# Kernel optimization log

Measured on AMD Instinct MI355X. Metric: run time of the kernel, lower is better.

## Reference

```python
import jax, jax.numpy as jnp
import numpy as np

BATCH, FIELD, EMB = 2048, 32, 64
LAYER_SIZES = [64, 64, 64]
OUT_DIM = 1
FINAL_DIM = sum(LAYER_SIZES)  # 192 (direct_connect=True, no splits)


def setup_inputs() -> dict:
    key = jax.random.key(0)
    ks = jax.random.split(key, 10)
    inp = {
        "x0": jax.random.normal(ks[0], (BATCH, FIELD, EMB), dtype=jnp.float32),
        # Conv1d(kernel_size=1) weights reshaped to (out, prev_field, field):
        "W1": jax.random.normal(ks[1], (LAYER_SIZES[0], FIELD, FIELD), dtype=jnp.float32) * 0.05,
        "b1": jax.random.normal(ks[2], (LAYER_SIZES[0],), dtype=jnp.float32) * 0.05,
        "W2": jax.random.normal(ks[3], (LAYER_SIZES[1], LAYER_SIZES[0], FIELD), dtype=jnp.float32) * 0.05,
        "b2": jax.random.normal(ks[4], (LAYER_SIZES[1],), dtype=jnp.float32) * 0.05,
        "W3": jax.random.normal(ks[5], (LAYER_SIZES[2], LAYER_SIZES[1], FIELD), dtype=jnp.float32) * 0.05,
        "b3": jax.random.normal(ks[6], (LAYER_SIZES[2],), dtype=jnp.float32) * 0.05,
        "W_out": jax.random.normal(ks[7], (FINAL_DIM, OUT_DIM), dtype=jnp.float32) * 0.05,
        "b_out": jax.random.normal(ks[8], (OUT_DIM,), dtype=jnp.float32) * 0.05,
    }
    return inp


def _cin_layer(W, b, xk, x0):
    # Fused: outer product einsum('bhd,bmd->bhmd') + reshape + 1x1 conv
    # == einsum over (prev_field h, field m) channel pair, per emb dim d.
    return jnp.einsum("ohm,bhd,bmd->bod", W, xk, x0) + b[None, :, None]


def reference(x0, W1, b1, W2, b2, W3, b3, W_out, b_out):
    # activation = identity; direct_connect = True (no splits, full carry)
    h1 = _cin_layer(W1, b1, x0, x0)   # (B, 64, D)
    h2 = _cin_layer(W2, b2, h1, x0)   # (B, 64, D)
    h3 = _cin_layer(W3, b3, h2, x0)   # (B, 64, D)
    stacked = jnp.concatenate([h1, h2, h3], axis=1)  # (B, 192, D)
    pooled = stacked.sum(axis=2)                     # (B, 192)
    return pooled @ W_out + b_out                    # (B, 1)
```

## Files before the change

kernel.cpp:

```cpp
#include <hip/hip_runtime.h>

typedef _Float16 f16;
typedef _Float16 f16x2 __attribute__((ext_vector_type(2)));
typedef __fp16 fp16x2 __attribute__((ext_vector_type(2)));
typedef _Float16 f16x8 __attribute__((ext_vector_type(8)));
typedef float f32x4 __attribute__((ext_vector_type(4)));
typedef unsigned int u32;

union U2 { u32 u; f16x2 h; fp16x2 h2; };
union AF { f16x8 v; u32 u[4]; };

__global__ __launch_bounds__(256) void pre_w3eff(
    const float* __restrict__ W3, const float* __restrict__ W_out,
    float* __restrict__ W3eff) {
    const int idx = blockIdx.x * 256 + threadIdx.x;
    float acc[8] = {0.f, 0.f, 0.f, 0.f, 0.f, 0.f, 0.f, 0.f};
#pragma unroll
    for (int ob = 0; ob < 8; ++ob)
#pragma unroll
        for (int oi = 0; oi < 8; ++oi) {
            int o = ob * 8 + oi;
            acc[oi] += W_out[128 + o] * W3[o * 2048 + idx];
        }
    float s = 0.f;
#pragma unroll
    for (int oi = 0; oi < 8; ++oi) s += acc[oi];
    W3eff[idx] = s;
}

__global__ __launch_bounds__(256) void pre_rest(
    const float* __restrict__ W1, const float* __restrict__ b1,
    const float* __restrict__ W2, const float* __restrict__ b2,
    const float* __restrict__ b3, const float* __restrict__ W_out,
    const float* __restrict__ b_out, const float* __restrict__ W3eff_g,
    f16* __restrict__ Wfrag, float* __restrict__ rvec, float* __restrict__ cnst) {
    const int blk = blockIdx.x, t = threadIdx.x;
    if (blk < 64) {
        const int h = blk;
        __shared__ float w3e[2048];
        __shared__ float w2s[2048];
        __shared__ float wo2[64];
#pragma unroll
        for (int i = 0; i < 8; ++i) {
            int idx = t + 256 * i;
            w3e[idx] = W3eff_g[idx];
            w2s[idx] = W2[((idx >> 5) * 64 + h) * 32 + (idx & 31)];
        }
        if (t < 64) wo2[t] = W_out[64 + t];
        __syncthreads();
        for (int idx = t; idx < 576; idx += 256) {
            int c = idx >> 5, kk = idx & 31;
            int sg = c >> 1, par = c & 1, A = kk >> 1, z = kk & 1;
            int B = (A + sg) & 15;
            float val = 0.f;
            if (sg == 0 && par == 1 && z == 1) {
                val = 0.f;
            } else if (sg == 8 && A >= 8) {
                int m = par ? (kk - 16) : kk;
                float s = 0.f;
#pragma unroll 8
                for (int o = 0; o < 64; ++o) s += wo2[o] * w2s[o * 32 + m];
                val = s;
            } else {
                int a = 2 * A + (par ? (1 - z) : z);
                int bq = 2 * B + z;
                float s = 0.f;
                if (a == bq) {
#pragma unroll 8
                    for (int o = 0; o < 64; ++o)
                        s += w3e[o * 32 + a] * w2s[o * 32 + a];
                } else {
#pragma unroll 8
                    for (int o = 0; o < 64; ++o)
                        s += w3e[o * 32 + bq] * w2s[o * 32 + a] +
                             w3e[o * 32 + a] * w2s[o * 32 + bq];
                }
                val = s;
            }
            int g = (kk >> 2) & 3, bb = (kk & 3) + 4 * (kk >> 4);
            int t4 = 4 + (h >> 4), l = 16 * g + (h & 15);
            Wfrag[((c * 8 + t4) * 64 + l) * 8 + bb] = (f16)val;
        }
    } else if (blk < 128) {
        const int h = blk - 64;
        __shared__ float w1r[1024];
        for (int i = t; i < 1024; i += 256) w1r[i] = W1[h * 1024 + i];
        __syncthreads();
        for (int idx = t; idx < 576; idx += 256) {
            int c = idx >> 5, kk = idx & 31;
            int sg = c >> 1, par = c & 1, A = kk >> 1, z = kk & 1;
            int B = (A + sg) & 15;
            float val = 0.f;
            if ((sg == 0 && par == 1 && z == 1) || (sg == 8 && A >= 8)) {
                val = 0.f;
            } else {
                int a = 2 * A + (par ? (1 - z) : z);
                int bq = 2 * B + z;
                val = (a == bq) ? w1r[33 * a] : (w1r[32 * a + bq] + w1r[32 * bq + a]);
            }
            int g = (kk >> 2) & 3, bb = (kk & 3) + 4 * (kk >> 4);
            int t4 = h >> 4, l = 16 * g + (h & 15);
            Wfrag[((c * 8 + t4) * 64 + l) * 8 + bb] = (f16)val;
        }
    } else {
        if (t < 32) {
            float acc[8] = {0.f, 0.f, 0.f, 0.f, 0.f, 0.f, 0.f, 0.f};
#pragma unroll
            for (int hb = 0; hb < 8; ++hb)
#pragma unroll
                for (int hi = 0; hi < 8; ++hi) {
                    int h = hb * 8 + hi;
                    acc[hi] += b2[h] * W3eff_g[h * 32 + t];
                }
            float r = 0.f;
#pragma unroll
            for (int hi = 0; hi < 8; ++hi) r += acc[hi];
            rvec[t] = r;
        }
        if (t >= 64 && t < 128) {
            int o = t - 64;
            float v = b1[o] * W_out[o] + b2[o] * W_out[64 + o] +
                      b3[o] * W_out[128 + o];
#pragma unroll
            for (int off = 32; off; off >>= 1) v += __shfl_xor(v, off);
            if (o == 0) cnst[0] = b_out[0] + 64.f * v;
        }
    }
}


#define EPOS(row, col) ((row) * 64 + (((col) + 4 * (row)) & 63))

__global__ __launch_bounds__(256, 3) void cin_main(
    const float* __restrict__ x0, const f16* __restrict__ Wfrag,
    const float* __restrict__ b1, const float* __restrict__ W_out,
    const float* __restrict__ rvec, const float* __restrict__ cnst,
    float* __restrict__ out) {
    __shared__ __align__(16) u32 FQ[2 * 32 * 130];
    __shared__ float eps[2][16 * 64];
    __shared__ float b1s[64], w1s[64], rs[32], rvb[2], obuf[2][2];

    const int t = threadIdx.x;
    const int w = t >> 6, lane = t & 63;
    const int wr = w >> 1, wc = w & 1;
    const int g = (lane >> 4) & 3, l15 = lane & 15;
    const int blk = blockIdx.x;

    {
        const float* src = x0 + (size_t)blk * 4096;
        const int J = t >> 4, l = t & 15;
        int r0 = 2 * J, r1 = 2 * J + 1, r2 = (2 * J + 2) & 31, r3 = (2 * J + 3) & 31;
#pragma unroll
        for (int bl = 0; bl < 2; ++bl) {
            const float* sb = src + bl * 2048;
#pragma unroll
            for (int k2 = 0; k2 < 4; ++k2) {
                int d = 16 * k2 + l;
                U2 u0, u1;
                u0.h2 = __builtin_amdgcn_cvt_pkrtz(sb[r0 * 64 + d], sb[r1 * 64 + d]);
                u1.h2 = __builtin_amdgcn_cvt_pkrtz(sb[r2 * 64 + d], sb[r3 * 64 + d]);
                uint2 ent; ent.x = u0.u; ent.y = u1.u;
                int base = bl * 4160 + J * 130 + 2 * d;
                *reinterpret_cast<uint2*>(&FQ[base]) = ent;
                *reinterpret_cast<uint2*>(&FQ[base + 2080]) = ent;
            }
        }
    }
    if (t < 64) { b1s[t] = b1[t]; w1s[t] = W_out[t]; }
    if (t >= 64 && t < 96) rs[t - 64] = rvec[t - 64];
    __syncthreads();

    const int v1base = wr * 4160 + 260 * g + 2 * l15;

    U2 xp[4][4], xpsw[4][4];
#pragma unroll
    for (int s = 0; s < 4; ++s) {
        uint2 qa = *reinterpret_cast<const uint2*>(&FQ[v1base + 32 * s]);
        uint2 qb = *reinterpret_cast<const uint2*>(&FQ[v1base + 32 * s + 1040]);
        xp[s][0].u = qa.x; xp[s][1].u = qa.y; xp[s][2].u = qb.x; xp[s][3].u = qb.y;
#pragma unroll
        for (int i = 0; i < 4; ++i)
            xpsw[s][i].u = (xp[s][i].u >> 16) | (xp[s][i].u << 16);
    }

    f32x4 acc[4][4];
#pragma unroll
    for (int s = 0; s < 4; ++s)
#pragma unroll
        for (int tt = 0; tt < 4; ++tt) acc[s][tt] = f32x4{0.f, 0.f, 0.f, 0.f};

    const f16x8* Wg = reinterpret_cast<const f16x8*>(Wfrag);
    f16x8 bfA[4], bfB[4];
#pragma unroll
    for (int tt = 0; tt < 4; ++tt) bfA[tt] = Wg[(wc * 4 + tt) * 64 + lane];

#define PKU(xa, ub) ({ U2 b_; b_.u = (ub); U2 r_; r_.h = (xa).h * b_.h; r_.u; })

#define PREF(dst, cc) { _Pragma("unroll") for (int tt = 0; tt < 4; ++tt) \
    dst[tt] = Wg[((cc) * 8 + wc * 4 + tt) * 64 + lane]; }

#define BODY(cc, bfr) { \
    _Pragma("unroll") \
    for (int s = 0; s < 4; ++s) { \
        AF af; \
        if ((cc) == 0) { \
            _Pragma("unroll") \
            for (int i = 0; i < 4; ++i) af.u[i] = PKU(xp[s][i], xp[s][i].u); \
        } else if ((cc) == 1) { \
            _Pragma("unroll") \
            for (int i = 0; i < 4; ++i) af.u[i] = PKU(xpsw[s][i], xp[s][i].u); \
        } else if ((cc) < 16) { \
            uint2 qa = *reinterpret_cast<const uint2*>(&FQ[v1base + 32 * s + ((cc) >> 1) * 130]); \
            uint2 qb = *reinterpret_cast<const uint2*>(&FQ[v1base + 32 * s + 1040 + ((cc) >> 1) * 130]); \
            if ((cc) & 1) { \
                af.u[0] = PKU(xpsw[s][0], qa.x); af.u[1] = PKU(xpsw[s][1], qa.y); \
                af.u[2] = PKU(xpsw[s][2], qb.x); af.u[3] = PKU(xpsw[s][3], qb.y); \
            } else { \
                af.u[0] = PKU(xp[s][0], qa.x); af.u[1] = PKU(xp[s][1], qa.y); \
                af.u[2] = PKU(xp[s][2], qb.x); af.u[3] = PKU(xp[s][3], qb.y); \
            } \
        } else if ((cc) == 16) { \
            uint2 qa = *reinterpret_cast<const uint2*>(&FQ[v1base + 32 * s + 1040]); \
            af.u[0] = PKU(xp[s][0], qa.x); af.u[1] = PKU(xp[s][1], qa.y); \
            af.u[2] = xp[s][2].u; af.u[3] = xp[s][3].u; \
        } else { \
            uint2 qa = *reinterpret_cast<const uint2*>(&FQ[v1base + 32 * s + 1040]); \
            af.u[0] = PKU(xpsw[s][0], qa.x); af.u[1] = PKU(xpsw[s][1], qa.y); \
            af.u[2] = xp[s][0].u; af.u[3] = xp[s][1].u; \
        } \
        __builtin_amdgcn_s_setprio(1); \
        _Pragma("unroll") \
        for (int tt = 0; tt < 4; ++tt) \
            acc[s][tt] = __builtin_amdgcn_mfma_f32_16x16x32_f16(af.v, bfr[tt], acc[s][tt], 0, 0, 0); \
        __builtin_amdgcn_s_setprio(0); \
    } }

    PREF(bfB, 1);  BODY(0, bfA);
    PREF(bfA, 2);  BODY(1, bfB);
    PREF(bfB, 3);  BODY(2, bfA);
    PREF(bfA, 4);  BODY(3, bfB);
    PREF(bfB, 5);  BODY(4, bfA);
    PREF(bfA, 6);  BODY(5, bfB);
    PREF(bfB, 7);  BODY(6, bfA);
    PREF(bfA, 8);  BODY(7, bfB);
    PREF(bfB, 9);  BODY(8, bfA);
    PREF(bfA, 10); BODY(9, bfB);
    PREF(bfB, 11); BODY(10, bfA);
    PREF(bfA, 12); BODY(11, bfB);
    PREF(bfB, 13); BODY(12, bfA);
    PREF(bfA, 14); BODY(13, bfB);
    PREF(bfB, 15); BODY(14, bfA);
    PREF(bfA, 16); BODY(15, bfB);
    PREF(bfB, 17); BODY(16, bfA);
    BODY(17, bfB);

#undef BODY
#undef PREF
#undef PKU

    if (wc == 0) {
        float sum = 0.f;
#pragma unroll
        for (int J = 0; J < 16; ++J) {
            U2 v; v.u = FQ[wr * 4160 + J * 130 + 2 * lane];
            sum += rs[2 * J] * (float)v.h[0] + rs[2 * J + 1] * (float)v.h[1];
        }
#pragma unroll
        for (int off = 32; off; off >>= 1) sum += __shfl_xor(sum, off);
        if (lane == 0) rvb[wr] = sum;
    }

    float bs = 0.f;
#pragma unroll
    for (int s = 0; s < 4; ++s) {
        if (wc == 1) {
#pragma unroll
            for (int tt = 0; tt < 4; ++tt) {
                float w1v = w1s[16 * tt + l15];
                float b1v = b1s[16 * tt + l15];
#pragma unroll
                for (int r = 0; r < 4; ++r) {
                    float a = acc[s][tt][r];
                    eps[wr][EPOS(4 * g + r, 16 * tt + l15)] = a + w1v;
                    bs += b1v * a;
                }
            }
        }
        __syncthreads();
        if (wc == 0) {
#pragma unroll
            for (int tt = 0; tt < 4; ++tt)
#pragma unroll
                for (int r = 0; r < 4; ++r)
                    bs += acc[s][tt][r] * eps[wr][EPOS(4 * g + r, 16 * tt + l15)];
        }
        __syncthreads();
    }
#pragma unroll
    for (int off = 32; off; off >>= 1) bs += __shfl_xor(bs, off);
    if (lane == 0) obuf[wr][wc] = bs;
    __syncthreads();
    if (t < 2)
        out[blk * 2 + t] = cnst[0] + rvb[t] + obuf[t][0] + obuf[t][1];
}

extern "C" void kernel_launch(void* const* d_in, const int* in_sizes, int n_in,
                              void* d_out, int out_size, void* d_ws, size_t ws_size,
                              hipStream_t stream) {
    const float* x0    = (const float*)d_in[0];
    const float* W1    = (const float*)d_in[1];
    const float* b1    = (const float*)d_in[2];
    const float* W2    = (const float*)d_in[3];
    const float* b2    = (const float*)d_in[4];
    const float* W3    = (const float*)d_in[5];
    const float* b3    = (const float*)d_in[6];
    const float* W_out = (const float*)d_in[7];
    const float* b_out = (const float*)d_in[8];

    char* wsb = (char*)d_ws;
    f16*   Wfrag = (f16*)wsb;
    float* W3effp = (float*)(wsb + 147456);
    float* rvecp = W3effp + 2048;
    float* cnstp = rvecp + 32;
    float* outp  = (float*)d_out;

    hipLaunchKernelGGL(pre_w3eff, dim3(8),   dim3(256), 0, stream, W3, W_out, W3effp);
    hipLaunchKernelGGL(pre_rest,  dim3(129), dim3(256), 0, stream,
                       W1, b1, W2, b2, b3, W_out, b_out, W3effp, Wfrag, rvecp, cnstp);
    hipLaunchKernelGGL(cin_main,  dim3(1024), dim3(256), 0, stream,
                       x0, Wfrag, b1, W_out, rvecp, cnstp, outp);
}
```

Measured before the change: 40.81 us.

## Process four batch rows per block and stage weight fragments via LDS DMA

Each block now handles four batch samples instead of two, so every loaded weight fragment feeds twice as many MFMAs. Weight chunks are double-buffered into shared memory with global_load_lds instead of per-thread register prefetch from global. The grid halves, occupancy drops to 2 blocks per SM, and a barrier is added after every chunk step. The aim is less weight-fetch traffic per sample, paid for with more registers (doubled accumulators), more barriers and fewer resident blocks.

```diff
diff --git a/kernel.cpp b/kernel.cpp
--- a/kernel.cpp
+++ b/kernel.cpp
@@ -129,16 +129,22 @@
 }
 
 
+__device__ __forceinline__ void gld16(const void* g, void* l) {
+    __builtin_amdgcn_global_load_lds(
+        (const __attribute__((address_space(1))) u32*)g,
+        (__attribute__((address_space(3))) u32*)l, 16, 0, 0);
+}
+
 #define EPOS(row, col) ((row) * 64 + (((col) + 4 * (row)) & 63))
 
-__global__ __launch_bounds__(256, 3) void cin_main(
+__global__ __launch_bounds__(256, 2) void cin_main(
     const float* __restrict__ x0, const f16* __restrict__ Wfrag,
     const float* __restrict__ b1, const float* __restrict__ W_out,
     const float* __restrict__ rvec, const float* __restrict__ cnst,
     float* __restrict__ out) {
-    __shared__ __align__(16) u32 FQ[2 * 32 * 130];
-    __shared__ float eps[2][16 * 64];
-    __shared__ float b1s[64], w1s[64], rs[32], rvb[2], obuf[2][2];
+    __shared__ __align__(16) u32 FQ[4 * 2080];
+    __shared__ __align__(16) char shB[16384];
+    __shared__ float b1s[64], w1s[64], rs[32], rvb[4], obuf[4][2];
 
     const int t = threadIdx.x;
     const int w = t >> 6, lane = t & 63;
@@ -146,23 +152,33 @@
     const int g = (lane >> 4) & 3, l15 = lane & 15;
     const int blk = blockIdx.x;
 
-    {
-        const float* src = x0 + (size_t)blk * 4096;
+    const char* WfB = reinterpret_cast<const char*>(Wfrag);
+
+#define STAGE(buf, ch)                                              \
+    do {                                                            \
+        const char* gs_ = WfB + (ch) * 8192 + w * 2048 + lane * 16; \
+        char* ls_ = shB + (buf) * 8192 + w * 2048;                  \
+        gld16(gs_, ls_);                                            \
+        gld16(gs_ + 1024, ls_ + 1024);                              \
+    } while (0)
+
+    STAGE(0, 0);
+
+    {
+        const float* src = x0 + (size_t)blk * 8192;
         const int J = t >> 4, l = t & 15;
-        int r0 = 2 * J, r1 = 2 * J + 1, r2 = (2 * J + 2) & 31, r3 = (2 * J + 3) & 31;
-#pragma unroll
-        for (int bl = 0; bl < 2; ++bl) {
+        int r0 = 2 * J, r1 = 2 * J + 1, r2_ = (2 * J + 2) & 31, r3_ = (2 * J + 3) & 31;
+#pragma unroll
+        for (int bl = 0; bl < 4; ++bl) {
             const float* sb = src + bl * 2048;
 #pragma unroll
             for (int k2 = 0; k2 < 4; ++k2) {
                 int d = 16 * k2 + l;
                 U2 u0, u1;
                 u0.h2 = __builtin_amdgcn_cvt_pkrtz(sb[r0 * 64 + d], sb[r1 * 64 + d]);
-                u1.h2 = __builtin_amdgcn_cvt_pkrtz(sb[r2 * 64 + d], sb[r3 * 64 + d]);
+                u1.h2 = __builtin_amdgcn_cvt_pkrtz(sb[r2_ * 64 + d], sb[r3_ * 64 + d]);
                 uint2 ent; ent.x = u0.u; ent.y = u1.u;
-                int base = bl * 4160 + J * 130 + 2 * d;
-                *reinterpret_cast<uint2*>(&FQ[base]) = ent;
-                *reinterpret_cast<uint2*>(&FQ[base + 2080]) = ent;
+                *reinterpret_cast<uint2*>(&FQ[bl * 2080 + J * 130 + 2 * d]) = ent;
             }
         }
     }
@@ -170,109 +186,143 @@
     if (t >= 64 && t < 96) rs[t - 64] = rvec[t - 64];
     __syncthreads();
 
-    const int v1base = wr * 4160 + 260 * g + 2 * l15;
-
-    U2 xp[4][4], xpsw[4][4];
-#pragma unroll
-    for (int s = 0; s < 4; ++s) {
-        uint2 qa = *reinterpret_cast<const uint2*>(&FQ[v1base + 32 * s]);
-        uint2 qb = *reinterpret_cast<const uint2*>(&FQ[v1base + 32 * s + 1040]);
+    const int fqA0 = (2 * wr) * 2080 + 260 * g + 2 * l15;
+    const int fqNB = (2 * wr) * 2080 + 2 * l15;
+
+    U2 xp[8][4], xpsw[8][4];
+#pragma unroll
+    for (int s = 0; s < 8; ++s) {
+        int fa = fqA0 + (s >> 2) * 2080 + 32 * (s & 3);
+        uint2 qa = *reinterpret_cast<const uint2*>(&FQ[fa]);
+        uint2 qb = *reinterpret_cast<const uint2*>(&FQ[fa + 1040]);
         xp[s][0].u = qa.x; xp[s][1].u = qa.y; xp[s][2].u = qb.x; xp[s][3].u = qb.y;
 #pragma unroll
         for (int i = 0; i < 4; ++i)
             xpsw[s][i].u = (xp[s][i].u >> 16) | (xp[s][i].u << 16);
     }
 
-    f32x4 acc[4][4];
-#pragma unroll
-    for (int s = 0; s < 4; ++s)
+    f32x4 acc[8][4];
+#pragma unroll
+    for (int s = 0; s < 8; ++s)
 #pragma unroll
         for (int tt = 0; tt < 4; ++tt) acc[s][tt] = f32x4{0.f, 0.f, 0.f, 0.f};
 
-    const f16x8* Wg = reinterpret_cast<const f16x8*>(Wfrag);
-    f16x8 bfA[4], bfB[4];
-#pragma unroll
-    for (int tt = 0; tt < 4; ++tt) bfA[tt] = Wg[(wc * 4 + tt) * 64 + lane];
-
 #define PKU(xa, ub) ({ U2 b_; b_.u = (ub); U2 r_; r_.h = (xa).h * b_.h; r_.u; })
 
-#define PREF(dst, cc) { _Pragma("unroll") for (int tt = 0; tt < 4; ++tt) \
-    dst[tt] = Wg[((cc) * 8 + wc * 4 + tt) * 64 + lane]; }
-
-#define BODY(cc, bfr) { \
-    _Pragma("unroll") \
-    for (int s = 0; s < 4; ++s) { \
-        AF af; \
-        if ((cc) == 0) { \
-            _Pragma("unroll") \
-            for (int i = 0; i < 4; ++i) af.u[i] = PKU(xp[s][i], xp[s][i].u); \
-        } else if ((cc) == 1) { \
-            _Pragma("unroll") \
-            for (int i = 0; i < 4; ++i) af.u[i] = PKU(xpsw[s][i], xp[s][i].u); \
-        } else if ((cc) < 16) { \
-            uint2 qa = *reinterpret_cast<const uint2*>(&FQ[v1base + 32 * s + ((cc) >> 1) * 130]); \
-            uint2 qb = *reinterpret_cast<const uint2*>(&FQ[v1base + 32 * s + 1040 + ((cc) >> 1) * 130]); \
-            if ((cc) & 1) { \
+#define LOADBF(bf, cc) { _Pragma("unroll") for (int tt = 0; tt < 4; ++tt) \
+    bf[tt] = *reinterpret_cast<const f16x8*>( \
+        shB + ((cc) & 1) * 8192 + ((wc * 4 + tt) * 64 + lane) * 16); }
+
+#define MFMA4(af, bf) { __builtin_amdgcn_s_setprio(1); \
+    _Pragma("unroll") for (int tt = 0; tt < 4; ++tt) \
+        acc[s][tt] = __builtin_amdgcn_mfma_f32_16x16x32_f16(af.v, bf[tt], acc[s][tt], 0, 0, 0); \
+    __builtin_amdgcn_s_setprio(0); }
+
+    STAGE(1, 1);
+    {
+        f16x8 bf[4]; LOADBF(bf, 0);
+#pragma unroll
+        for (int s = 0; s < 8; ++s) {
+            AF af;
+#pragma unroll
+            for (int i = 0; i < 4; ++i) af.u[i] = PKU(xp[s][i], xp[s][i].u);
+            MFMA4(af, bf);
+        }
+    }
+    __syncthreads();
+    STAGE(0, 2);
+    {
+        f16x8 bf[4]; LOADBF(bf, 1);
+#pragma unroll
+        for (int s = 0; s < 8; ++s) {
+            AF af;
+#pragma unroll
+            for (int i = 0; i < 4; ++i) af.u[i] = PKU(xpsw[s][i], xp[s][i].u);
+            MFMA4(af, bf);
+        }
+    }
+    __syncthreads();
+
+#define BODYG(cc)                                                             \
+    {                                                                         \
+        const int sg_ = (cc) >> 1;                                            \
+        const int rb_ = ((2 * g + 8 + sg_) & 15) * 130;                       \
+        f16x8 bf[4]; LOADBF(bf, cc);                                          \
+        _Pragma("unroll")                                                     \
+        for (int s = 0; s < 8; ++s) {                                         \
+            int fa = fqA0 + (s >> 2) * 2080 + sg_ * 130 + 32 * (s & 3);       \
+            int fb = fqNB + (s >> 2) * 2080 + rb_ + 32 * (s & 3);             \
+            uint2 qa = *reinterpret_cast<const uint2*>(&FQ[fa]);              \
+            uint2 qb = *reinterpret_cast<const uint2*>(&FQ[fb]);              \
+            AF af;                                                            \
+            if ((cc) & 1) {                                                   \
                 af.u[0] = PKU(xpsw[s][0], qa.x); af.u[1] = PKU(xpsw[s][1], qa.y); \
                 af.u[2] = PKU(xpsw[s][2], qb.x); af.u[3] = PKU(xpsw[s][3], qb.y); \
-            } else { \
+            } else {                                                          \
                 af.u[0] = PKU(xp[s][0], qa.x); af.u[1] = PKU(xp[s][1], qa.y); \
                 af.u[2] = PKU(xp[s][2], qb.x); af.u[3] = PKU(xp[s][3], qb.y); \
-            } \
-        } else if ((cc) == 16) { \
-            uint2 qa = *reinterpret_cast<const uint2*>(&FQ[v1base + 32 * s + 1040]); \
-            af.u[0] = PKU(xp[s][0], qa.x); af.u[1] = PKU(xp[s][1], qa.y); \
-            af.u[2] = xp[s][2].u; af.u[3] = xp[s][3].u; \
-        } else { \
-            uint2 qa = *reinterpret_cast<const uint2*>(&FQ[v1base + 32 * s + 1040]); \
-            af.u[0] = PKU(xpsw[s][0], qa.x); af.u[1] = PKU(xpsw[s][1], qa.y); \
-            af.u[2] = xp[s][0].u; af.u[3] = xp[s][1].u; \
-        } \
-        __builtin_amdgcn_s_setprio(1); \
-        _Pragma("unroll") \
-        for (int tt = 0; tt < 4; ++tt) \
-            acc[s][tt] = __builtin_amdgcn_mfma_f32_16x16x32_f16(af.v, bfr[tt], acc[s][tt], 0, 0, 0); \
-        __builtin_amdgcn_s_setprio(0); \
-    } }
-
-    PREF(bfB, 1);  BODY(0, bfA);
-    PREF(bfA, 2);  BODY(1, bfB);
-    PREF(bfB, 3);  BODY(2, bfA);
-    PREF(bfA, 4);  BODY(3, bfB);
-    PREF(bfB, 5);  BODY(4, bfA);
-    PREF(bfA, 6);  BODY(5, bfB);
-    PREF(bfB, 7);  BODY(6, bfA);
-    PREF(bfA, 8);  BODY(7, bfB);
-    PREF(bfB, 9);  BODY(8, bfA);
-    PREF(bfA, 10); BODY(9, bfB);
-    PREF(bfB, 11); BODY(10, bfA);
-    PREF(bfA, 12); BODY(11, bfB);
-    PREF(bfB, 13); BODY(12, bfA);
-    PREF(bfA, 14); BODY(13, bfB);
-    PREF(bfB, 15); BODY(14, bfA);
-    PREF(bfA, 16); BODY(15, bfB);
-    PREF(bfB, 17); BODY(16, bfA);
-    BODY(17, bfB);
-
-#undef BODY
-#undef PREF
+            }                                                                 \
+            MFMA4(af, bf);                                                    \
+        }                                                                     \
+    }
+
+#define STEP(cc) { STAGE(((cc) + 1) & 1, (cc) + 1); BODYG(cc); __syncthreads(); }
+
+    STEP(2);  STEP(3);  STEP(4);  STEP(5);  STEP(6);  STEP(7);
+    STEP(8);  STEP(9);  STEP(10); STEP(11); STEP(12); STEP(13);
+    STEP(14); STEP(15);
+
+    STAGE(1, 17);
+    {
+        f16x8 bf[4]; LOADBF(bf, 16);
+#pragma unroll
+        for (int s = 0; s < 8; ++s) {
+            int fa = fqA0 + (s >> 2) * 2080 + 1040 + 32 * (s & 3);
+            uint2 qa = *reinterpret_cast<const uint2*>(&FQ[fa]);
+            AF af;
+            af.u[0] = PKU(xp[s][0], qa.x); af.u[1] = PKU(xp[s][1], qa.y);
+            af.u[2] = xp[s][2].u; af.u[3] = xp[s][3].u;
+            MFMA4(af, bf);
+        }
+    }
+    __syncthreads();
+    {
+        f16x8 bf[4]; LOADBF(bf, 17);
+#pragma unroll
+        for (int s = 0; s < 8; ++s) {
+            int fa = fqA0 + (s >> 2) * 2080 + 1040 + 32 * (s & 3);
+            uint2 qa = *reinterpret_cast<const uint2*>(&FQ[fa]);
+            AF af;
+            af.u[0] = PKU(xpsw[s][0], qa.x); af.u[1] = PKU(xpsw[s][1], qa.y);
+            af.u[2] = xp[s][0].u; af.u[3] = xp[s][1].u;
+            MFMA4(af, bf);
+        }
+    }
+    __syncthreads();
+
+#undef STEP
+#undef BODYG
+#undef MFMA4
+#undef LOADBF
 #undef PKU
-
-    if (wc == 0) {
+#undef STAGE
+
+    {
         float sum = 0.f;
 #pragma unroll
         for (int J = 0; J < 16; ++J) {
-            U2 v; v.u = FQ[wr * 4160 + J * 130 + 2 * lane];
+            U2 v; v.u = FQ[w * 2080 + J * 130 + 2 * lane];
             sum += rs[2 * J] * (float)v.h[0] + rs[2 * J + 1] * (float)v.h[1];
         }
 #pragma unroll
         for (int off = 32; off; off >>= 1) sum += __shfl_xor(sum, off);
-        if (lane == 0) rvb[wr] = sum;
-    }
-
-    float bs = 0.f;
-#pragma unroll
-    for (int s = 0; s < 4; ++s) {
+        if (lane == 0) rvb[w] = sum;
+    }
+
+    float* eps = reinterpret_cast<float*>(shB);
+    float bs0 = 0.f, bs1 = 0.f;
+#pragma unroll
+    for (int s = 0; s < 8; ++s) {
         if (wc == 1) {
 #pragma unroll
             for (int tt = 0; tt < 4; ++tt) {
@@ -281,8 +331,9 @@
 #pragma unroll
                 for (int r = 0; r < 4; ++r) {
                     float a = acc[s][tt][r];
-                    eps[wr][EPOS(4 * g + r, 16 * tt + l15)] = a + w1v;
-                    bs += b1v * a;
+                    eps[wr * 1024 + EPOS(4 * g + r, 16 * tt + l15)] = a + w1v;
+                    float term = b1v * a;
+                    if (s < 4) bs0 += term; else bs1 += term;
                 }
             }
         }
@@ -291,17 +342,27 @@
 #pragma unroll
             for (int tt = 0; tt < 4; ++tt)
 #pragma unroll
-                for (int r = 0; r < 4; ++r)
-                    bs += acc[s][tt][r] * eps[wr][EPOS(4 * g + r, 16 * tt + l15)];
+                for (int r = 0; r < 4; ++r) {
+                    float term = acc[s][tt][r] *
+                                 eps[wr * 1024 + EPOS(4 * g + r, 16 * tt + l15)];
+                    if (s < 4) bs0 += term; else bs1 += term;
+                }
         }
         __syncthreads();
     }
 #pragma unroll
-    for (int off = 32; off; off >>= 1) bs += __shfl_xor(bs, off);
-    if (lane == 0) obuf[wr][wc] = bs;
-    __syncthreads();
-    if (t < 2)
-        out[blk * 2 + t] = cnst[0] + rvb[t] + obuf[t][0] + obuf[t][1];
+    for (int off = 32; off; off >>= 1) {
+        bs0 += __shfl_xor(bs0, off);
+        bs1 += __shfl_xor(bs1, off);
+    }
+    if (lane == 0) { obuf[w][0] = bs0; obuf[w][1] = bs1; }
+    __syncthreads();
+    if (t < 4) {
+        int bt = t;
+        out[blk * 4 + bt] = cnst[0] + rvb[bt] +
+                            obuf[2 * (bt >> 1) + 0][bt & 1] +
+                            obuf[2 * (bt >> 1) + 1][bt & 1];
+    }
 }
 
 extern "C" void kernel_launch(void* const* d_in, const int* in_sizes, int n_in,
@@ -327,6 +388,6 @@
     hipLaunchKernelGGL(pre_w3eff, dim3(8),   dim3(256), 0, stream, W3, W_out, W3effp);
     hipLaunchKernelGGL(pre_rest,  dim3(129), dim3(256), 0, stream,
                        W1, b1, W2, b2, b3, W_out, b_out, W3effp, Wfrag, rvecp, cnstp);
-    hipLaunchKernelGGL(cin_main,  dim3(1024), dim3(256), 0, stream,
+    hipLaunchKernelGGL(cin_main,  dim3(512), dim3(256), 0, stream,
                        x0, Wfrag, b1, W_out, rvecp, cnstp, outp);
 }
```

New measurement: 41.29 us. Within noise of the previous version (+1.2%).
